# Optimization experiments

Hardware: AMD Instinct MI355X
Metric: run time of the kernel (lower is better)

The kernel has to match this reference:

```python
import jax, jax.numpy as jnp
import numpy as np

B, S, E, H, Dh = 2, 2048, 1024, 16, 64


def setup_inputs() -> dict:
    key = jax.random.key(0)
    ks = jax.random.split(key, 8)
    w = 0.02
    return {
        "x": jax.random.normal(ks[0], (B, S, E), jnp.float32),
        # torch Linear convention: weight (out, in) = (Dh, E), stacked over heads
        "Wq": jax.random.normal(ks[1], (H, Dh, E), jnp.float32) * w,
        "bq": jax.random.normal(ks[2], (H, Dh), jnp.float32) * w,
        "Wk": jax.random.normal(ks[3], (H, Dh, E), jnp.float32) * w,
        "bk": jax.random.normal(ks[4], (H, Dh), jnp.float32) * w,
        "Wv": jax.random.normal(ks[5], (H, Dh, E), jnp.float32) * w,
        "bv": jax.random.normal(ks[6], (H, Dh), jnp.float32) * w,
        "proj": jax.random.normal(ks[7], (H * Dh, E), jnp.float32) * w,
    }


def reference(x, Wq, bq, Wk, bk, Wv, bv, proj):
    b, s, e = x.shape
    h, dh, _ = Wq.shape
    scale = jnp.sqrt(jnp.asarray(dh, x.dtype))
    # per-head linear projections: y = x @ W.T + b  -> (b, h, s, dh)
    q = jnp.einsum('bse,hde->bhsd', x, Wq) + bq[None, :, None, :]
    k = jnp.einsum('bse,hde->bhsd', x, Wk) + bk[None, :, None, :]
    v = jnp.einsum('bse,hde->bhsd', x, Wv) + bv[None, :, None, :]
    causal = jnp.triu(jnp.ones((s, s), bool), 1)
    scores = jnp.einsum('bhsd,bhtd->bhst', q, k) / scale
    scores = jnp.where(causal[None, None], -jnp.inf, scores)
    # quirk: softmax output divided by sqrt(head_size) a second time
    att = jax.nn.softmax(scores, axis=-1) / scale
    z = jnp.einsum('bhst,bhtd->bhsd', att, v)
    # quirk: torch reshapes (B,H,S,Dh) row-major into (B,S,H*Dh) WITHOUT transpose
    z = z.reshape(b, s, h * dh)
    return z @ proj
```

## Files before the change

### kernel.cpp

```cpp
#include <hip/hip_runtime.h>
#include <hip/hip_bf16.h>

typedef unsigned short u16;
typedef unsigned int u32;
typedef __bf16 bf16x8 __attribute__((ext_vector_type(8)));
typedef float f32x4 __attribute__((ext_vector_type(4)));
typedef u16 u16x8 __attribute__((ext_vector_type(8)));
typedef u16 u16x4 __attribute__((ext_vector_type(4)));
typedef u32 u32x4 __attribute__((ext_vector_type(4)));

#define B_ 2
#define S_ 2048
#define E_ 1024
#define H_ 16
#define Dh_ 64

static __device__ __forceinline__ u16 f2bf(float f) {
  unsigned u = __builtin_bit_cast(unsigned, f);
  u += 0x7fff + ((u >> 16) & 1);
  return (u16)(u >> 16);
}

static __device__ __forceinline__ void gload16(const u16* g, u16* l) {
  __builtin_amdgcn_global_load_lds((const __attribute__((address_space(1))) unsigned int*)g,
                                   (__attribute__((address_space(3))) unsigned int*)l,
                                   16, 0, 0);
}

__global__ void cvt_all(const float* __restrict__ x, const float* __restrict__ wq,
                        const float* __restrict__ wk, const float* __restrict__ wv,
                        const float* __restrict__ proj,
                        u16* __restrict__ xb, u16* __restrict__ wcat, u16* __restrict__ pjt) {
  __shared__ float tt[32][33];
  const int bid = blockIdx.x;
  const int tid = threadIdx.x;
  if (bid < 3584) {
    const int i = bid * 256 + tid;
    const float* src; u16x8* dst;
    if (i < 524288) {
      src = x + (size_t)i * 8;            dst = (u16x8*)xb + i;
    } else {
      const int j = i - 524288;
      dst = (u16x8*)wcat + j;
      if (j < 131072)      src = wq + (size_t)j * 8;
      else if (j < 262144) src = wk + (size_t)(j - 131072) * 8;
      else                 src = wv + (size_t)(j - 262144) * 8;
    }
    float4 a = ((const float4*)src)[0], b = ((const float4*)src)[1];
    u16x8 o;
    o[0] = f2bf(a.x); o[1] = f2bf(a.y); o[2] = f2bf(a.z); o[3] = f2bf(a.w);
    o[4] = f2bf(b.x); o[5] = f2bf(b.y); o[6] = f2bf(b.z); o[7] = f2bf(b.w);
    *dst = o;
  } else {
    const int tb = bid - 3584;
    const int e0 = (tb & 31) * 32, f0 = (tb >> 5) * 32;
    const int tx = tid & 31, ty = tid >> 5;
#pragma unroll
    for (int r = 0; r < 4; ++r) {
      const int row = ty + r * 8;
      tt[row][tx] = proj[(f0 + row) * 1024 + e0 + tx];
    }
    __syncthreads();
#pragma unroll
    for (int r = 0; r < 4; ++r) {
      const int row = ty + r * 8;
      pjt[(e0 + row) * 1024 + f0 + tx] = f2bf(tt[tx][row]);
    }
  }
}

__global__ __launch_bounds__(512, 2) void qkv_gemm(const u16* __restrict__ Wcat,
                                                   const u16* __restrict__ Xm,
                                                   const float* __restrict__ bq,
                                                   const float* __restrict__ bk,
                                                   const float* __restrict__ bv,
                                                   u16* __restrict__ Qb, u16* __restrict__ Kb,
                                                   u16* __restrict__ Vtb, float qs) {
  __shared__ __align__(16) u16 Alds[2][12288];
  __shared__ __align__(16) u16 Blds[2][16384];
  const int tid = threadIdx.x;
  const int wv = tid >> 6, ln = tid & 63;
  const int lq = ln & 15, lg = ln >> 4;
  const int wm = wv >> 2, wn = wv & 3;
  const int bid = blockIdx.x;
  const int xcd = bid & 7, w = bid >> 3;
  const int bx = w & 15;
  const int by = xcd * 2 + (w >> 4);
  const int ra0 = bx * 192, rb0 = by * 256;

  const int r_t = tid >> 3, c_t = tid & 7;
  const int gcol = (c_t ^ (r_t & 7)) * 8;
  const u16* Asrc = Wcat + (ra0 + r_t) * 1024 + gcol;
  const u16* Bsrc = Xm   + (rb0 + r_t) * 1024 + gcol;

  const int sc0 = (lg ^ (lq & 7)) * 8;
  const int sc1 = ((4 + lg) ^ (lq & 7)) * 8;
  const int baseA = (wm * 96 + lq) * 64;
  const int baseB = (wn * 64 + lq) * 64;

  f32x4 acc[6][4];
  const f32x4 z4 = {0.f, 0.f, 0.f, 0.f};
#pragma unroll
  for (int i = 0; i < 6; ++i)
#pragma unroll
    for (int j = 0; j < 4; ++j) acc[i][j] = z4;

#define SA(G, KT, BUF) gload16(Asrc + (G) * 65536 + (KT) * 64, &Alds[BUF][((G) * 512 + tid) * 8])
#define SB(G, KT, BUF) gload16(Bsrc + (G) * 65536 + (KT) * 64, &Blds[BUF][((G) * 512 + tid) * 8])
#define LOADA(MH, SC) do {                                                         \
    _Pragma("unroll") for (int ii = 0; ii < 3; ++ii)                               \
      af[ii] = *(const bf16x8*)&Alds[cb][baseA + (MH) * 3072 + ii * 1024 + (SC)];  \
  } while (0)
#define LOADB(DST, SC) do {                                                        \
    _Pragma("unroll") for (int j = 0; j < 4; ++j)                                  \
      DST[j] = *(const bf16x8*)&Blds[cb][baseB + j * 1024 + (SC)];                 \
  } while (0)
#define MF(MH, BQ) do {                                                            \
    _Pragma("unroll") for (int ii = 0; ii < 3; ++ii)                               \
      _Pragma("unroll") for (int j = 0; j < 4; ++j)                                \
        acc[(MH) * 3 + ii][j] =                                                    \
            __builtin_amdgcn_mfma_f32_16x16x32_bf16(af[ii], BQ[j],                 \
                                                    acc[(MH) * 3 + ii][j], 0, 0, 0); \
  } while (0)

  SB(0, 0, 0); SB(1, 0, 0); SB(2, 0, 0); SB(3, 0, 0);
  SA(0, 0, 0); SA(1, 0, 0); SA(2, 0, 0);

  for (int kt = 0; kt < 16; ++kt) {
    const int cb = kt & 1, nb = cb ^ 1;
    const bool st = (kt < 15);
    asm volatile("s_waitcnt vmcnt(0)" ::: "memory");
    __builtin_amdgcn_s_barrier();
    __builtin_amdgcn_sched_barrier(0);
    bf16x8 af[3], bq0[4], bq1[4];
    LOADA(0, sc0);
    LOADB(bq0, sc0);
    if (st) { SB(0, kt + 1, nb); SB(1, kt + 1, nb); }
    __builtin_amdgcn_s_barrier();
    asm volatile("s_waitcnt lgkmcnt(0)" ::: "memory");
    __builtin_amdgcn_sched_barrier(0);
    __builtin_amdgcn_s_setprio(1);
    MF(0, bq0);
    __builtin_amdgcn_s_setprio(0);
    __builtin_amdgcn_s_barrier();
    LOADA(0, sc1);
    LOADB(bq1, sc1);
    if (st) { SB(2, kt + 1, nb); SB(3, kt + 1, nb); }
    __builtin_amdgcn_s_barrier();
    asm volatile("s_waitcnt lgkmcnt(0)" ::: "memory");
    __builtin_amdgcn_sched_barrier(0);
    __builtin_amdgcn_s_setprio(1);
    MF(0, bq1);
    __builtin_amdgcn_s_setprio(0);
    __builtin_amdgcn_s_barrier();
    LOADA(1, sc0);
    if (st) { SA(0, kt + 1, nb); SA(1, kt + 1, nb); }
    __builtin_amdgcn_s_barrier();
    asm volatile("s_waitcnt lgkmcnt(0)" ::: "memory");
    __builtin_amdgcn_sched_barrier(0);
    __builtin_amdgcn_s_setprio(1);
    MF(1, bq0);
    __builtin_amdgcn_s_setprio(0);
    __builtin_amdgcn_s_barrier();
    LOADA(1, sc1);
    if (st) { SA(2, kt + 1, nb); }
    __builtin_amdgcn_s_barrier();
    asm volatile("s_waitcnt lgkmcnt(0)" ::: "memory");
    __builtin_amdgcn_sched_barrier(0);
    __builtin_amdgcn_s_setprio(1);
    MF(1, bq1);
    __builtin_amdgcn_s_setprio(0);
    __builtin_amdgcn_s_barrier();
  }
#undef SA
#undef SB
#undef LOADA
#undef LOADB
#undef MF

#pragma unroll
  for (int i = 0; i < 6; ++i) {
    const int n0 = ra0 + wm * 96 + i * 16 + lg * 4;
    const int reg_i = n0 >> 10;
    const int nl = n0 & 1023;
    const int h = nl >> 6, d = nl & 63;
    const float* bias = (reg_i == 0) ? bq : (reg_i == 1) ? bk : bv;
    const float osc = (reg_i == 0) ? qs : 1.0f;
    const float4 b4 = *(const float4*)&bias[nl];
#pragma unroll
    for (int j = 0; j < 4; ++j) {
      const int m = rb0 + wn * 64 + j * 16 + lq;
      const int bb = m >> 11, s = m & 2047;
      if (reg_i < 2) {
        u16* out = (reg_i == 0) ? Qb : Kb;
        u16x4 pk;
        pk[0] = f2bf((acc[i][j][0] + b4.x) * osc);
        pk[1] = f2bf((acc[i][j][1] + b4.y) * osc);
        pk[2] = f2bf((acc[i][j][2] + b4.z) * osc);
        pk[3] = f2bf((acc[i][j][3] + b4.w) * osc);
        *(u16x4*)&out[((bb * H_ + h) * S_ + s) * Dh_ + d] = pk;
      } else {
        const float bvv[4] = {b4.x, b4.y, b4.z, b4.w};
#pragma unroll
        for (int r = 0; r < 4; ++r)
          Vtb[((bb * H_ + h) * Dh_ + d + r) * S_ + s] = f2bf(acc[i][j][r] + bvv[r]);
      }
    }
  }
}

__global__ __launch_bounds__(512, 2) void proj_gemm(const u16* __restrict__ Am,
                                                    const u16* __restrict__ Bm,
                                                    float* __restrict__ out) {
  __shared__ __align__(16) u16 Alds[2][8192];
  __shared__ __align__(16) u16 Blds[2][8192];
  const int tid = threadIdx.x;
  const int wv = tid >> 6, ln = tid & 63;
  const int lq = ln & 15, lg = ln >> 4;
  const int wm = wv >> 2, wn = wv & 3;
  const int bid = blockIdx.x;
  const int xcd = bid & 7, w = bid >> 3;
  const int bx = w & 7;
  const int by = xcd * 4 + (w >> 3);
  const int ra0 = bx * 128, rb0 = by * 128;

  const int r_t = tid >> 3, c_t = tid & 7;
  const int gcol = (c_t ^ (r_t & 7)) * 8;
  const u16* Asrc = Am + (ra0 + r_t) * 1024 + gcol;
  const u16* Bsrc = Bm + (rb0 + r_t) * 1024 + gcol;

  const int sc0 = (lg ^ (lq & 7)) * 8;
  const int sc1 = ((4 + lg) ^ (lq & 7)) * 8;
  const int baseA = (wm * 64 + lq) * 64;
  const int baseB = (wn * 32 + lq) * 64;

  f32x4 acc[4][2];
  const f32x4 z4 = {0.f, 0.f, 0.f, 0.f};
#pragma unroll
  for (int i = 0; i < 4; ++i)
#pragma unroll
    for (int j = 0; j < 2; ++j) acc[i][j] = z4;

#define SA(G, KT, BUF) gload16(Asrc + (G) * 65536 + (KT) * 64, &Alds[BUF][((G) * 512 + tid) * 8])
#define SB(G, KT, BUF) gload16(Bsrc + (G) * 65536 + (KT) * 64, &Blds[BUF][((G) * 512 + tid) * 8])
#define LOADAB(SC) do {                                                            \
    _Pragma("unroll") for (int ii = 0; ii < 4; ++ii)                               \
      af[ii] = *(const bf16x8*)&Alds[cb][baseA + ii * 1024 + (SC)];                \
    _Pragma("unroll") for (int j = 0; j < 2; ++j)                                  \
      bf[j] = *(const bf16x8*)&Blds[cb][baseB + j * 1024 + (SC)];                  \
  } while (0)
#define MF() do {                                                                  \
    _Pragma("unroll") for (int ii = 0; ii < 4; ++ii)                               \
      _Pragma("unroll") for (int j = 0; j < 2; ++j)                                \
        acc[ii][j] = __builtin_amdgcn_mfma_f32_16x16x32_bf16(af[ii], bf[j],        \
                                                             acc[ii][j], 0, 0, 0); \
  } while (0)

  SA(0, 0, 0); SA(1, 0, 0); SB(0, 0, 0); SB(1, 0, 0);

  for (int kt = 0; kt < 16; ++kt) {
    const int cb = kt & 1, nb = cb ^ 1;
    const bool st = (kt < 15);
    asm volatile("s_waitcnt vmcnt(0)" ::: "memory");
    __builtin_amdgcn_s_barrier();
    __builtin_amdgcn_sched_barrier(0);
    bf16x8 af[4], bf[2];
    LOADAB(sc0);
    if (st) { SA(0, kt + 1, nb); SA(1, kt + 1, nb); }
    __builtin_amdgcn_s_barrier();
    asm volatile("s_waitcnt lgkmcnt(0)" ::: "memory");
    __builtin_amdgcn_sched_barrier(0);
    __builtin_amdgcn_s_setprio(1);
    MF();
    __builtin_amdgcn_s_setprio(0);
    __builtin_amdgcn_s_barrier();
    LOADAB(sc1);
    if (st) { SB(0, kt + 1, nb); SB(1, kt + 1, nb); }
    __builtin_amdgcn_s_barrier();
    asm volatile("s_waitcnt lgkmcnt(0)" ::: "memory");
    __builtin_amdgcn_sched_barrier(0);
    __builtin_amdgcn_s_setprio(1);
    MF();
    __builtin_amdgcn_s_setprio(0);
    __builtin_amdgcn_s_barrier();
  }
#undef SA
#undef SB
#undef LOADAB
#undef MF

#pragma unroll
  for (int i = 0; i < 4; ++i)
#pragma unroll
    for (int j = 0; j < 2; ++j) {
      const int e0 = ra0 + wm * 64 + i * 16 + lg * 4;
      const int m = rb0 + wn * 32 + j * 16 + lq;
      *(f32x4*)&out[m * 1024 + e0] = acc[i][j];
    }
}

__global__ __launch_bounds__(512, 4) void attn_kernel(const u16* __restrict__ Q,
                                                      const u16* __restrict__ K,
                                                      const u16* __restrict__ Vt,
                                                      u16* __restrict__ Z) {
  __shared__ __align__(16) u16 Ktile[2][8192];
  __shared__ __align__(16) u16 Vtile[2][8192];
  const int tid = threadIdx.x;
  const int wv = tid >> 6, ln = tid & 63;
  const int lq = ln & 15, lg = ln >> 4;
  const bool lgodd = (lg & 1) != 0;
  const int id = blockIdx.x;
  const int within = id >> 3;
  const int xg = id & 7;
  int bh, qt;
  if (within < 32) { bh = xg * 4 + (within >> 4);     qt = 15 - (within & 15); }
  else { const int w = within - 32; bh = xg * 4 + 2 + (w >> 4); qt = w & 15; }
  const int qrow = (qt << 7) + wv * 16 + lq;
  const u16* Qp = Q + (size_t)bh * S_ * Dh_;
  const u16* Kp = K + (size_t)bh * S_ * Dh_;
  const u16* Vp = Vt + (size_t)bh * Dh_ * S_;

  int kgofs[2], vgrow[2], vgcol[2];
#pragma unroll
  for (int j = 0; j < 2; ++j) {
    const int p = j * 512 + tid;
    const int gk = p ^ ((p >> 3) & 7);
    kgofs[j] = (gk >> 3) * 64 + (gk & 7) * 8;
    vgrow[j] = p >> 4;
    vgcol[j] = ((p & 15) ^ ((p >> 4) & 15)) * 8;
  }
  const int sc0 = (lg ^ (lq & 7)) * 8;
  const int sc1 = ((4 + lg) ^ (lq & 7)) * 8;

  bf16x8 qf0 = *(const bf16x8*)&Qp[qrow * Dh_ + lg * 8];
  bf16x8 qf1 = *(const bf16x8*)&Qp[qrow * Dh_ + 32 + lg * 8];

  f32x4 o[4];
  const f32x4 z4 = {0.f, 0.f, 0.f, 0.f};
#pragma unroll
  for (int dt = 0; dt < 4; ++dt) o[dt] = z4;
  float l_lane = 0.f;

#define STAGE(KT, BUF) do { const int kb_ = (KT) * 128;                              \
    gload16(Kp + (size_t)kb_ * 64 + kgofs[0], &Ktile[BUF][wv * 512]);                \
    gload16(Kp + (size_t)kb_ * 64 + kgofs[1], &Ktile[BUF][4096 + wv * 512]);         \
    gload16(Vp + (size_t)vgrow[0] * 2048 + kb_ + vgcol[0], &Vtile[BUF][wv * 512]);   \
    gload16(Vp + (size_t)vgrow[1] * 2048 + kb_ + vgcol[1], &Vtile[BUF][4096 + wv * 512]); \
  } while (0)

  STAGE(0, 0);

  int cur = 0;
  for (int kt = 0; kt <= qt; ++kt) {
    asm volatile("s_waitcnt vmcnt(0)" ::: "memory");
    __builtin_amdgcn_s_barrier();
    __builtin_amdgcn_sched_barrier(0);
    if (kt < qt) STAGE(kt + 1, cur ^ 1);
    const int k0 = kt * 128;
    const bool diag = (kt == qt);
    const int nkk = diag ? ((wv >> 1) + 1) : 4;

    f32x4 sa[4], sb[4];
    __builtin_amdgcn_s_setprio(1);
#pragma unroll
    for (int kk = 0; kk < 4; ++kk) {
      if (kk < nkk) {
        const int rA = (kk * 32 + lq) * 64;
        const int rB = rA + 1024;
        bf16x8 kA0 = *(const bf16x8*)&Ktile[cur][rA + sc0];
        bf16x8 kA1 = *(const bf16x8*)&Ktile[cur][rA + sc1];
        bf16x8 kB0 = *(const bf16x8*)&Ktile[cur][rB + sc0];
        bf16x8 kB1 = *(const bf16x8*)&Ktile[cur][rB + sc1];
        f32x4 a = z4, b = z4;
        a = __builtin_amdgcn_mfma_f32_16x16x32_bf16(kA0, qf0, a, 0, 0, 0);
        a = __builtin_amdgcn_mfma_f32_16x16x32_bf16(kA1, qf1, a, 0, 0, 0);
        b = __builtin_amdgcn_mfma_f32_16x16x32_bf16(kB0, qf0, b, 0, 0, 0);
        b = __builtin_amdgcn_mfma_f32_16x16x32_bf16(kB1, qf1, b, 0, 0, 0);
        sa[kk] = a; sb[kk] = b;
      }
    }
    __builtin_amdgcn_s_setprio(0);

#pragma unroll
    for (int kk = 0; kk < 4; ++kk) {
      if (kk < nkk) {
        f32x4 xa = sa[kk], xb = sb[kk];
        if (diag) {
          const int keyA = k0 + kk * 32 + lg * 4;
          const int keyB = keyA + 16;
#pragma unroll
          for (int r = 0; r < 4; ++r) {
            if (keyA + r > qrow) xa[r] = -3.0e38f;
            if (keyB + r > qrow) xb[r] = -3.0e38f;
          }
        }
        float e0 = __builtin_amdgcn_exp2f(xa[0]);
        float e1 = __builtin_amdgcn_exp2f(xa[1]);
        float e2 = __builtin_amdgcn_exp2f(xa[2]);
        float e3 = __builtin_amdgcn_exp2f(xa[3]);
        float f0 = __builtin_amdgcn_exp2f(xb[0]);
        float f1 = __builtin_amdgcn_exp2f(xb[1]);
        float f2 = __builtin_amdgcn_exp2f(xb[2]);
        float f3 = __builtin_amdgcn_exp2f(xb[3]);
        l_lane += ((e0 + e1) + (e2 + e3)) + ((f0 + f1) + (f2 + f3));
        u32 A0, A1, B0, B1;
        asm("v_cvt_pk_bf16_f32 %0, %1, %2" : "=v"(A0) : "v"(e0), "v"(e1));
        asm("v_cvt_pk_bf16_f32 %0, %1, %2" : "=v"(A1) : "v"(e2), "v"(e3));
        asm("v_cvt_pk_bf16_f32 %0, %1, %2" : "=v"(B0) : "v"(f0), "v"(f1));
        asm("v_cvt_pk_bf16_f32 %0, %1, %2" : "=v"(B1) : "v"(f2), "v"(f3));
        asm("v_permlane32_swap_b32 %0, %1" : "+v"(A0), "+v"(B0));
        asm("v_permlane32_swap_b32 %0, %1" : "+v"(A1), "+v"(B1));
        const u32 A0x = __shfl_xor((int)A0, 16), B0x = __shfl_xor((int)B0, 16);
        const u32 A1x = __shfl_xor((int)A1, 16), B1x = __shfl_xor((int)B1, 16);
        u32x4 w;
        w[0] = lgodd ? B0x : A0;
        w[1] = lgodd ? B1x : A1;
        w[2] = lgodd ? B0 : A0x;
        w[3] = lgodd ? B1 : A1x;
        const bf16x8 pf = __builtin_bit_cast(bf16x8, w);
        const int scvk = ((kk * 4 + lg) ^ lq) * 8;
        __builtin_amdgcn_s_setprio(1);
#pragma unroll
        for (int dt = 0; dt < 4; ++dt) {
          bf16x8 vf = *(const bf16x8*)&Vtile[cur][(dt * 16 + lq) * 128 + scvk];
          o[dt] = __builtin_amdgcn_mfma_f32_16x16x32_bf16(vf, pf, o[dt], 0, 0, 0);
        }
        __builtin_amdgcn_s_setprio(0);
      }
    }
    cur ^= 1;
  }
#undef STAGE

  float l = l_lane;
  l += __shfl_xor(l, 16);
  l += __shfl_xor(l, 32);
  const float inv = 0.125f / l;
#pragma unroll
  for (int dt = 0; dt < 4; ++dt) {
    u16x4 pko;
#pragma unroll
    for (int r = 0; r < 4; ++r) pko[r] = f2bf(o[dt][r] * inv);
    *(u16x4*)&Z[((size_t)bh * S_ + qrow) * Dh_ + dt * 16 + lg * 4] = pko;
  }
}

extern "C" void kernel_launch(void* const* d_in, const int* in_sizes, int n_in,
                              void* d_out, int out_size, void* d_ws, size_t ws_size,
                              hipStream_t stream) {
  const float* x    = (const float*)d_in[0];
  const float* Wq   = (const float*)d_in[1];
  const float* bq   = (const float*)d_in[2];
  const float* Wk   = (const float*)d_in[3];
  const float* bk   = (const float*)d_in[4];
  const float* Wv   = (const float*)d_in[5];
  const float* bv   = (const float*)d_in[6];
  const float* proj = (const float*)d_in[7];
  float* out = (float*)d_out;

  char* p = (char*)d_ws;
  u16* xb   = (u16*)p; p += (size_t)4096 * 1024 * 2;
  u16* wcat = (u16*)p; p += (size_t)3072 * 1024 * 2;
  u16* pjt  = (u16*)p; p += (size_t)1024 * 1024 * 2;
  u16* Qb   = (u16*)p; p += (size_t)4096 * 1024 * 2;
  u16* Kb   = (u16*)p; p += (size_t)4096 * 1024 * 2;
  u16* Vtb  = (u16*)p; p += (size_t)4096 * 1024 * 2;
  u16* Zb   = (u16*)p; p += (size_t)4096 * 1024 * 2;

  cvt_all<<<dim3(4608), dim3(256), 0, stream>>>(x, Wq, Wk, Wv, proj, xb, wcat, pjt);

  const float qs = 0.125f * 1.44269504f;
  qkv_gemm<<<dim3(256), dim3(512), 0, stream>>>(wcat, xb, bq, bk, bv, Qb, Kb, Vtb, qs);

  attn_kernel<<<dim3(512), dim3(512), 0, stream>>>(Qb, Kb, Vtb, Zb);

  proj_gemm<<<dim3(256), dim3(512), 0, stream>>>(pjt, Zb, out);
}
```

Baseline: 97.70 us.

## Halve QKV GEMM N-tile to 128 and double grid for more occupancy

The QKV projection GEMM tile shrinks from 192x256 to 192x128, so the grid grows from 256 to 512 blocks and launch bounds allow 4 blocks per CU. The K-step pipeline is reorganised from four sub-phases into two, with each phase loading all six A fragments and two B fragments. The goal is better CU coverage and latency hiding on a grid that previously only covered 256 CUs. In exchange, arithmetic intensity per tile drops and the weight matrix is reloaded more often. Higher register and LDS pressure per CU may also limit the occupancy actually reached.

```diff
diff --git a/kernel.cpp b/kernel.cpp
--- a/kernel.cpp
+++ b/kernel.cpp
@@ -69,7 +69,7 @@
   }
 }
 
-__global__ __launch_bounds__(512, 2) void qkv_gemm(const u16* __restrict__ Wcat,
+__global__ __launch_bounds__(512, 4) void qkv_gemm(const u16* __restrict__ Wcat,
                                                    const u16* __restrict__ Xm,
                                                    const float* __restrict__ bq,
                                                    const float* __restrict__ bk,
@@ -77,7 +77,7 @@
                                                    u16* __restrict__ Qb, u16* __restrict__ Kb,
                                                    u16* __restrict__ Vtb, float qs) {
   __shared__ __align__(16) u16 Alds[2][12288];
-  __shared__ __align__(16) u16 Blds[2][16384];
+  __shared__ __align__(16) u16 Blds[2][8192];
   const int tid = threadIdx.x;
   const int wv = tid >> 6, ln = tid & 63;
   const int lq = ln & 15, lg = ln >> 4;
@@ -85,8 +85,8 @@
   const int bid = blockIdx.x;
   const int xcd = bid & 7, w = bid >> 3;
   const int bx = w & 15;
-  const int by = xcd * 2 + (w >> 4);
-  const int ra0 = bx * 192, rb0 = by * 256;
+  const int by = xcd * 4 + (w >> 4);
+  const int ra0 = bx * 192, rb0 = by * 128;
 
   const int r_t = tid >> 3, c_t = tid & 7;
   const int gcol = (c_t ^ (r_t & 7)) * 8;
@@ -96,35 +96,31 @@
   const int sc0 = (lg ^ (lq & 7)) * 8;
   const int sc1 = ((4 + lg) ^ (lq & 7)) * 8;
   const int baseA = (wm * 96 + lq) * 64;
-  const int baseB = (wn * 64 + lq) * 64;
-
-  f32x4 acc[6][4];
+  const int baseB = (wn * 32 + lq) * 64;
+
+  f32x4 acc[6][2];
   const f32x4 z4 = {0.f, 0.f, 0.f, 0.f};
 #pragma unroll
   for (int i = 0; i < 6; ++i)
 #pragma unroll
-    for (int j = 0; j < 4; ++j) acc[i][j] = z4;
+    for (int j = 0; j < 2; ++j) acc[i][j] = z4;
 
 #define SA(G, KT, BUF) gload16(Asrc + (G) * 65536 + (KT) * 64, &Alds[BUF][((G) * 512 + tid) * 8])
 #define SB(G, KT, BUF) gload16(Bsrc + (G) * 65536 + (KT) * 64, &Blds[BUF][((G) * 512 + tid) * 8])
-#define LOADA(MH, SC) do {                                                         \
-    _Pragma("unroll") for (int ii = 0; ii < 3; ++ii)                               \
-      af[ii] = *(const bf16x8*)&Alds[cb][baseA + (MH) * 3072 + ii * 1024 + (SC)];  \
+#define LOADAB(SC) do {                                                            \
+    _Pragma("unroll") for (int ii = 0; ii < 6; ++ii)                               \
+      af[ii] = *(const bf16x8*)&Alds[cb][baseA + ii * 1024 + (SC)];                \
+    _Pragma("unroll") for (int j = 0; j < 2; ++j)                                  \
+      bfr[j] = *(const bf16x8*)&Blds[cb][baseB + j * 1024 + (SC)];                 \
   } while (0)
-#define LOADB(DST, SC) do {                                                        \
-    _Pragma("unroll") for (int j = 0; j < 4; ++j)                                  \
-      DST[j] = *(const bf16x8*)&Blds[cb][baseB + j * 1024 + (SC)];                 \
+#define MF() do {                                                                  \
+    _Pragma("unroll") for (int ii = 0; ii < 6; ++ii)                               \
+      _Pragma("unroll") for (int j = 0; j < 2; ++j)                                \
+        acc[ii][j] = __builtin_amdgcn_mfma_f32_16x16x32_bf16(af[ii], bfr[j],       \
+                                                             acc[ii][j], 0, 0, 0); \
   } while (0)
-#define MF(MH, BQ) do {                                                            \
-    _Pragma("unroll") for (int ii = 0; ii < 3; ++ii)                               \
-      _Pragma("unroll") for (int j = 0; j < 4; ++j)                                \
-        acc[(MH) * 3 + ii][j] =                                                    \
-            __builtin_amdgcn_mfma_f32_16x16x32_bf16(af[ii], BQ[j],                 \
-                                                    acc[(MH) * 3 + ii][j], 0, 0, 0); \
-  } while (0)
-
-  SB(0, 0, 0); SB(1, 0, 0); SB(2, 0, 0); SB(3, 0, 0);
-  SA(0, 0, 0); SA(1, 0, 0); SA(2, 0, 0);
+
+  SA(0, 0, 0); SA(1, 0, 0); SA(2, 0, 0); SB(0, 0, 0); SB(1, 0, 0);
 
   for (int kt = 0; kt < 16; ++kt) {
     const int cb = kt & 1, nb = cb ^ 1;
@@ -132,50 +128,29 @@
     asm volatile("s_waitcnt vmcnt(0)" ::: "memory");
     __builtin_amdgcn_s_barrier();
     __builtin_amdgcn_sched_barrier(0);
-    bf16x8 af[3], bq0[4], bq1[4];
-    LOADA(0, sc0);
-    LOADB(bq0, sc0);
+    bf16x8 af[6], bfr[2];
+    LOADAB(sc0);
+    if (st) { SA(0, kt + 1, nb); SA(1, kt + 1, nb); SA(2, kt + 1, nb); }
+    __builtin_amdgcn_s_barrier();
+    asm volatile("s_waitcnt lgkmcnt(0)" ::: "memory");
+    __builtin_amdgcn_sched_barrier(0);
+    __builtin_amdgcn_s_setprio(1);
+    MF();
+    __builtin_amdgcn_s_setprio(0);
+    __builtin_amdgcn_s_barrier();
+    LOADAB(sc1);
     if (st) { SB(0, kt + 1, nb); SB(1, kt + 1, nb); }
     __builtin_amdgcn_s_barrier();
     asm volatile("s_waitcnt lgkmcnt(0)" ::: "memory");
     __builtin_amdgcn_sched_barrier(0);
     __builtin_amdgcn_s_setprio(1);
-    MF(0, bq0);
-    __builtin_amdgcn_s_setprio(0);
-    __builtin_amdgcn_s_barrier();
-    LOADA(0, sc1);
-    LOADB(bq1, sc1);
-    if (st) { SB(2, kt + 1, nb); SB(3, kt + 1, nb); }
-    __builtin_amdgcn_s_barrier();
-    asm volatile("s_waitcnt lgkmcnt(0)" ::: "memory");
-    __builtin_amdgcn_sched_barrier(0);
-    __builtin_amdgcn_s_setprio(1);
-    MF(0, bq1);
-    __builtin_amdgcn_s_setprio(0);
-    __builtin_amdgcn_s_barrier();
-    LOADA(1, sc0);
-    if (st) { SA(0, kt + 1, nb); SA(1, kt + 1, nb); }
-    __builtin_amdgcn_s_barrier();
-    asm volatile("s_waitcnt lgkmcnt(0)" ::: "memory");
-    __builtin_amdgcn_sched_barrier(0);
-    __builtin_amdgcn_s_setprio(1);
-    MF(1, bq0);
-    __builtin_amdgcn_s_setprio(0);
-    __builtin_amdgcn_s_barrier();
-    LOADA(1, sc1);
-    if (st) { SA(2, kt + 1, nb); }
-    __builtin_amdgcn_s_barrier();
-    asm volatile("s_waitcnt lgkmcnt(0)" ::: "memory");
-    __builtin_amdgcn_sched_barrier(0);
-    __builtin_amdgcn_s_setprio(1);
-    MF(1, bq1);
+    MF();
     __builtin_amdgcn_s_setprio(0);
     __builtin_amdgcn_s_barrier();
   }
 #undef SA
 #undef SB
-#undef LOADA
-#undef LOADB
+#undef LOADAB
 #undef MF
 
 #pragma unroll
@@ -188,8 +163,8 @@
     const float osc = (reg_i == 0) ? qs : 1.0f;
     const float4 b4 = *(const float4*)&bias[nl];
 #pragma unroll
-    for (int j = 0; j < 4; ++j) {
-      const int m = rb0 + wn * 64 + j * 16 + lq;
+    for (int j = 0; j < 2; ++j) {
+      const int m = rb0 + wn * 32 + j * 16 + lq;
       const int bb = m >> 11, s = m & 2047;
       if (reg_i < 2) {
         u16* out = (reg_i == 0) ? Qb : Kb;
@@ -470,7 +445,7 @@
   cvt_all<<<dim3(4608), dim3(256), 0, stream>>>(x, Wq, Wk, Wv, proj, xb, wcat, pjt);
 
   const float qs = 0.125f * 1.44269504f;
-  qkv_gemm<<<dim3(256), dim3(512), 0, stream>>>(wcat, xb, bq, bk, bv, Qb, Kb, Vtb, qs);
+  qkv_gemm<<<dim3(512), dim3(512), 0, stream>>>(wcat, xb, bq, bk, bv, Qb, Kb, Vtb, qs);
 
   attn_kernel<<<dim3(512), dim3(512), 0, stream>>>(Qb, Kb, Vtb, Zb);
 
```

New measurement: 95.73 us. -2.0%, faster.
